# Kernel tuning notes

Hardware: AMD Instinct MI355X
Metric: run time of the kernel (lower is better)

The kernel has to match this reference:

```python
import jax, jax.numpy as jnp
import numpy as np

B, N, D_IN, D_OUT = 4, 4096, 512, 256
ALPHA = 0.2          # LeakyReLU negative slope
NEG_BIG = -9e15      # value used to mask non-edges before softmax


def setup_inputs() -> dict:
    key = jax.random.key(0)
    k_h, k_adj, k_w, k_a = jax.random.split(key, 4)
    h = jax.random.normal(k_h, (B, N, D_IN), dtype=jnp.float32)
    adj = jax.random.randint(k_adj, (N, N), 0, 2, dtype=jnp.int32)
    # xavier_uniform with gain 1.414
    lim_w = 1.414 * np.sqrt(6.0 / (D_IN + D_OUT))
    Ws = jax.random.uniform(k_w, (B, D_IN, D_OUT), jnp.float32, -lim_w, lim_w)
    lim_a = 1.414 * np.sqrt(6.0 / (2 * D_OUT + 1))
    a = jax.random.uniform(k_a, (B, 2 * D_OUT, 1), jnp.float32, -lim_a, lim_a)
    return {"h": h, "adj": adj, "Ws": Ws, "a": a}


def reference(h, adj, Ws, a):
    d_out = Ws.shape[-1]
    Wh = jnp.einsum('bni,bio->bno', h, Ws)                 # [B,N,D_OUT]
    a1 = a[:, :d_out, 0]                                    # [B,D_OUT]
    a2 = a[:, d_out:, 0]                                    # [B,D_OUT]
    e1 = jnp.einsum('bno,bo->bn', Wh, a1)                   # [B,N]
    e2 = jnp.einsum('bno,bo->bn', Wh, a2)                   # [B,N]
    e = e1[:, :, None] + e2[:, None, :]                     # [B,N,N]
    e = jnp.where(e > 0, e, ALPHA * e)                      # LeakyReLU
    scores = jnp.where(adj[None, :, :] > 0, e, NEG_BIG)     # mask non-edges
    att = jax.nn.softmax(scores, axis=-1)                   # over neighbors j
    # dropout omitted (eval mode / p irrelevant for correctness baseline)
    h_prime = jnp.einsum('bnm,bmo->bno', att, Wh)           # [B,N,D_OUT]
    return jax.nn.elu(h_prime)                              # concat=True -> elu
```

## Files before the change

### kernel.cpp

```cpp
#include <hip/hip_runtime.h>
#include <hip/hip_bf16.h>
#include <stdint.h>

#define B_    4
#define NN    4096
#define DIN   512
#define DOUT  256
#define ALPHA_ 0.2f

typedef __attribute__((ext_vector_type(8))) short short8;
typedef __attribute__((ext_vector_type(4))) float f32x4;
typedef __attribute__((ext_vector_type(2))) float f32x2;

typedef const __attribute__((address_space(1))) void gconst_void;
typedef __attribute__((address_space(3))) void lds_void;

__device__ __forceinline__ unsigned short f2bf(float x) {
    union { float f; uint32_t u; } v; v.f = x;
    uint32_t r = v.u + 0x7FFFu + ((v.u >> 16) & 1u);
    return (unsigned short)(r >> 16);
}

__global__ __launch_bounds__(256) void k_prep(const int* __restrict__ adj,
                                              const float4* __restrict__ h4,
                                              const float* __restrict__ Ws,
                                              uint32_t* __restrict__ bits,
                                              uint2* __restrict__ hb,
                                              unsigned short* __restrict__ wst) {
    const int gt = blockIdx.x * 256 + threadIdx.x;
    const int NT = 2048 * 256;
    for (int idx = gt; idx < NN * NN; idx += NT) {
        unsigned long long m = __ballot(adj[idx] > 0);
        if ((threadIdx.x & 63) == 0)
            *reinterpret_cast<unsigned long long*>(bits + ((idx >> 6) << 1)) = m;
    }
    for (int idx = gt; idx < B_ * NN * DIN / 4; idx += NT) {
        float4 v = h4[idx];
        uint2 o;
        o.x = (uint32_t)f2bf(v.x) | ((uint32_t)f2bf(v.y) << 16);
        o.y = (uint32_t)f2bf(v.z) | ((uint32_t)f2bf(v.w) << 16);
        hb[idx] = o;
    }
    for (int idx = gt; idx < B_ * DOUT * DIN; idx += NT) {
        int k = idx & (DIN - 1);
        int o = (idx >> 9) & (DOUT - 1);
        int b = idx >> 17;
        wst[idx] = f2bf(Ws[((size_t)b * DIN + k) * DOUT + o]);
    }
}

__global__ __launch_bounds__(256) void k_gemm1(const unsigned short* __restrict__ hb,
                                               const unsigned short* __restrict__ wst,
                                               const float* __restrict__ a,
                                               unsigned short* __restrict__ wht,
                                               float2* __restrict__ x1t,
                                               float* __restrict__ y1t,
                                               float* __restrict__ y2t) {
    __shared__ unsigned short Ah[64 * 64];
    __shared__ unsigned short Bw[256 * 64];
    __shared__ float e1s[64], e2s[64];
    const int tid = threadIdx.x;
    const int w = tid >> 6, lane = tid & 63;
    const int l15 = lane & 15, lhi = lane >> 4;
    const int b = blockIdx.y;
    const int n0 = blockIdx.x * 64;
    const unsigned short* hrow = hb + ((size_t)b * NN + n0) * DIN;
    const unsigned short* wrow = wst + (size_t)b * DOUT * DIN;

    if (tid < 64) { e1s[tid] = 0.f; e2s[tid] = 0.f; }

    f32x4 acc[4][4] = {};

    for (int kt = 0; kt < DIN / 64; ++kt) {
        const int k0 = kt * 64;
        #pragma unroll
        for (int it = 0; it < 2; ++it) {
            int q = it * 256 + tid;
            int row = q >> 3, c = q & 7;
            const unsigned short* src = hrow + (size_t)row * DIN + k0 + 8 * (c ^ (row & 7));
            char* dst = reinterpret_cast<char*>(Ah) + it * 4096 + w * 1024;
            __builtin_amdgcn_global_load_lds((gconst_void*)src, (lds_void*)dst, 16, 0, 0);
        }
        #pragma unroll
        for (int it = 0; it < 8; ++it) {
            int q = it * 256 + tid;
            int row = q >> 3, c = q & 7;
            const unsigned short* src = wrow + (size_t)row * DIN + k0 + 8 * (c ^ (row & 7));
            char* dst = reinterpret_cast<char*>(Bw) + it * 4096 + w * 1024;
            __builtin_amdgcn_global_load_lds((gconst_void*)src, (lds_void*)dst, 16, 0, 0);
        }
        __syncthreads();
        #pragma unroll
        for (int kk = 0; kk < 2; ++kk) {
            short8 af[4], bfr[4];
            #pragma unroll
            for (int rf = 0; rf < 4; ++rf) {
                int row = rf * 16 + l15;
                int off = row * 128 + ((kk * 64 + lhi * 16) ^ ((row & 7) << 4));
                af[rf] = *reinterpret_cast<const short8*>(reinterpret_cast<const char*>(Ah) + off);
            }
            #pragma unroll
            for (int cf = 0; cf < 4; ++cf) {
                int row = w * 64 + cf * 16 + l15;
                int off = row * 128 + ((kk * 64 + lhi * 16) ^ ((row & 7) << 4));
                bfr[cf] = *reinterpret_cast<const short8*>(reinterpret_cast<const char*>(Bw) + off);
            }
            #pragma unroll
            for (int rf = 0; rf < 4; ++rf)
                #pragma unroll
                for (int cf = 0; cf < 4; ++cf)
                    acc[rf][cf] = __builtin_amdgcn_mfma_f32_16x16x32_bf16(af[rf], bfr[cf], acc[rf][cf], 0, 0, 0);
        }
        __syncthreads();
    }
    unsigned short* wb = wht + (size_t)b * DOUT * NN;
    #pragma unroll
    for (int rf = 0; rf < 4; ++rf) {
        #pragma unroll
        for (int cf = 0; cf < 4; ++cf) {
            int d = w * 64 + cf * 16 + l15;
            int m = n0 + rf * 16 + lhi * 4;
            uint2 pk;
            pk.x = (uint32_t)f2bf(acc[rf][cf][0]) | ((uint32_t)f2bf(acc[rf][cf][1]) << 16);
            pk.y = (uint32_t)f2bf(acc[rf][cf][2]) | ((uint32_t)f2bf(acc[rf][cf][3]) << 16);
            *reinterpret_cast<uint2*>(wb + (size_t)d * NN + m) = pk;
        }
    }
    const float* ab = a + b * 2 * DOUT;
    float a1v[4], a2v[4];
    #pragma unroll
    for (int cf = 0; cf < 4; ++cf) {
        int d = w * 64 + cf * 16 + l15;
        a1v[cf] = ab[d];
        a2v[cf] = ab[DOUT + d];
    }
    #pragma unroll
    for (int rf = 0; rf < 4; ++rf) {
        #pragma unroll
        for (int j = 0; j < 4; ++j) {
            float p1 = 0.f, p2 = 0.f;
            #pragma unroll
            for (int cf = 0; cf < 4; ++cf) {
                p1 = fmaf(acc[rf][cf][j], a1v[cf], p1);
                p2 = fmaf(acc[rf][cf][j], a2v[cf], p2);
            }
            #pragma unroll
            for (int msk = 1; msk < 16; msk <<= 1) {
                p1 += __shfl_xor(p1, msk);
                p2 += __shfl_xor(p2, msk);
            }
            if (l15 == 0) {
                atomicAdd(&e1s[rf * 16 + lhi * 4 + j], p1);
                atomicAdd(&e2s[rf * 16 + lhi * 4 + j], p2);
            }
        }
    }
    __syncthreads();
    if (tid < 64) {
        float e1v = e1s[tid], e2v = e2s[tid];
        x1t[b * NN + n0 + tid] = float2{__expf(e1v), __expf(ALPHA_ * e1v)};
        y1t[b * NN + n0 + tid] = __expf(e2v);
        y2t[b * NN + n0 + tid] = __expf(ALPHA_ * e2v);
    }
}

__global__ __launch_bounds__(512, 4) void k_attn(const unsigned short* __restrict__ wht,
                                                 const uint32_t* __restrict__ bits,
                                                 const float2* __restrict__ x1t,
                                                 const float* __restrict__ y1t,
                                                 const float* __restrict__ y2t,
                                                 float* __restrict__ out,
                                                 float* __restrict__ part1,
                                                 float* __restrict__ sums0,
                                                 float* __restrict__ sums1) {
    __shared__ unsigned short Bw[2 * 256 * 64];
    __shared__ unsigned short Pt[2 * 64 * 64];

    const int tid = threadIdx.x;
    const int w = tid >> 6, lane = tid & 63;
    const int l15 = lane & 15, lh4 = lane >> 4;
    const int wn = w >> 2, wd = w & 3;

    const int bid = blockIdx.x;
    const int wg = ((bid & 7) << 6) | (bid >> 3);
    const int g  = wg >> 6;
    const int b  = g >> 1;
    const int n0 = ((g & 1) * 32 + (wg & 31)) << 6;
    const int T0 = ((wg >> 5) & 1) * 32;

    const int pr = tid >> 3, pc = tid & 7;
    const float2 xv = x1t[b * NN + n0 + pr];
    const float X1 = xv.x, X2 = xv.y;
    const unsigned short* wb = wht + (size_t)b * DOUT * NN;

    f32x4 acc[2][4] = {};
    f32x4 accs[2] = {};
    short8 ones;
    {
        union { short8 v; uint32_t u[4]; } ov;
        ov.u[0] = 0x3F803F80u; ov.u[1] = 0x3F803F80u;
        ov.u[2] = 0x3F803F80u; ov.u[3] = 0x3F803F80u;
        ones = ov.v;
    }

    const unsigned short* sp[4];
    #pragma unroll
    for (int it = 0; it < 4; ++it) {
        int q = it * 512 + tid;
        int row = q >> 3, c = q & 7;
        sp[it] = wb + (size_t)row * NN + T0 * 64 + 8 * (c ^ (row & 7));
    }
    const uint8_t* bp = reinterpret_cast<const uint8_t*>(bits) +
                        (size_t)(n0 + pr) * (NN / 8) + T0 * 8 + pc;
    const float4* y1p = reinterpret_cast<const float4*>(y1t + b * NN + T0 * 64 + pc * 8);
    const float4* y2p = reinterpret_cast<const float4*>(y2t + b * NN + T0 * 64 + pc * 8);

#define STAGE(BUF)                                                                     \
    {                                                                                  \
        _Pragma("unroll")                                                              \
        for (int it = 0; it < 4; ++it) {                                               \
            char* dst = reinterpret_cast<char*>(Bw) + (BUF) * 32768 + it * 8192 + w * 1024; \
            __builtin_amdgcn_global_load_lds((gconst_void*)sp[it], (lds_void*)dst, 16, 0, 0); \
            sp[it] += 64;                                                              \
        }                                                                              \
    }

#define P_MATH(BB, Y1A, Y1B, Y2A, Y2B, PKW)                                            \
    {                                                                                  \
        float v1[8] = {Y1A.x, Y1A.y, Y1A.z, Y1A.w, Y1B.x, Y1B.y, Y1B.z, Y1B.w};        \
        float v2[8] = {Y2A.x, Y2A.y, Y2A.z, Y2A.w, Y2B.x, Y2B.y, Y2B.z, Y2B.w};        \
        _Pragma("unroll")                                                              \
        for (int i = 0; i < 4; ++i) {                                                  \
            f32x2 pa = f32x2{v1[2 * i], v1[2 * i + 1]} * X1;                           \
            f32x2 pb = f32x2{v2[2 * i], v2[2 * i + 1]} * X2;                           \
            f32x2 pm = __builtin_elementwise_max(pa, pb);                              \
            union { __hip_bfloat162 h; uint32_t u; } cc;                               \
            cc.h = __float22bfloat162_rn(float2{pm.x, pm.y});                          \
            uint32_t b2 = ((BB) >> (2 * i)) & 3u;                                      \
            uint32_t mk = ((b2 & 1u) ? 0xFFFFu : 0u) | ((b2 & 2u) ? 0xFFFF0000u : 0u); \
            PKW[i] = cc.u & mk;                                                        \
        }                                                                              \
    }

#define PT_WRITE(PKW, BUF)                                                             \
    {                                                                                  \
        uint4 qv; qv.x = PKW[0]; qv.y = PKW[1]; qv.z = PKW[2]; qv.w = PKW[3];          \
        *reinterpret_cast<uint4*>(reinterpret_cast<char*>(Pt) + (BUF) * 8192 +         \
                                  pr * 128 + ((pc * 16) ^ ((pr & 7) << 4))) = qv;      \
    }

#define MM(CUR)                                                                        \
    {                                                                                  \
        const char* bwb = reinterpret_cast<const char*>(Bw) + (CUR) * 32768;           \
        const char* ptb = reinterpret_cast<const char*>(Pt) + (CUR) * 8192;            \
        __builtin_amdgcn_s_setprio(1);                                                 \
        _Pragma("unroll")                                                              \
        for (int kk = 0; kk < 2; ++kk) {                                               \
            short8 af[2], bf[4];                                                       \
            _Pragma("unroll")                                                          \
            for (int rf = 0; rf < 2; ++rf) {                                           \
                int row = wn * 32 + rf * 16 + l15;                                     \
                int off = row * 128 + ((kk * 64 + lh4 * 16) ^ ((row & 7) << 4));       \
                af[rf] = *reinterpret_cast<const short8*>(ptb + off);                  \
            }                                                                          \
            _Pragma("unroll")                                                          \
            for (int cf = 0; cf < 4; ++cf) {                                           \
                int row = wd * 64 + cf * 16 + l15;                                     \
                int off = row * 128 + ((kk * 64 + lh4 * 16) ^ ((row & 7) << 4));       \
                bf[cf] = *reinterpret_cast<const short8*>(bwb + off);                  \
            }                                                                          \
            _Pragma("unroll")                                                          \
            for (int rf = 0; rf < 2; ++rf) {                                           \
                _Pragma("unroll")                                                      \
                for (int cf = 0; cf < 4; ++cf)                                         \
                    acc[rf][cf] = __builtin_amdgcn_mfma_f32_16x16x32_bf16(             \
                        af[rf], bf[cf], acc[rf][cf], 0, 0, 0);                         \
                accs[rf] = __builtin_amdgcn_mfma_f32_16x16x32_bf16(                    \
                    af[rf], ones, accs[rf], 0, 0, 0);                                  \
            }                                                                          \
        }                                                                              \
        __builtin_amdgcn_s_setprio(0);                                                 \
    }

    STAGE(0)
    {
        uint32_t bb = *bp; bp += 8;
        float4 y1a = y1p[0], y1b = y1p[1]; y1p += 16;
        float4 y2a = y2p[0], y2b = y2p[1]; y2p += 16;
        uint32_t pkw[4];
        P_MATH(bb, y1a, y1b, y2a, y2b, pkw)
        PT_WRITE(pkw, 0)
    }
    __syncthreads();

    for (int t = 0; t < 32; ++t) {
        const int cur = t & 1;
        if (t < 31) {
            STAGE(cur ^ 1)
            uint32_t bb = *bp; bp += 8;
            float4 y1a = y1p[0], y1b = y1p[1]; y1p += 16;
            float4 y2a = y2p[0], y2b = y2p[1]; y2p += 16;
            uint32_t pkw[4];
            P_MATH(bb, y1a, y1b, y2a, y2b, pkw)
            PT_WRITE(pkw, cur ^ 1)
        }
        MM(cur)
        __syncthreads();
    }
#undef STAGE
#undef P_MATH
#undef PT_WRITE
#undef MM

    float* pdst = (T0 == 0) ? out : part1;
    #pragma unroll
    for (int rf = 0; rf < 2; ++rf) {
        #pragma unroll
        for (int cf = 0; cf < 4; ++cf) {
            int d = wd * 64 + cf * 16 + l15;
            #pragma unroll
            for (int j = 0; j < 4; ++j) {
                int nr = n0 + wn * 32 + rf * 16 + lh4 * 4 + j;
                pdst[((size_t)b * NN + nr) * DOUT + d] = acc[rf][cf][j];
            }
        }
    }
    if (wd == 0 && l15 == 0) {
        float* sdst = (T0 == 0) ? sums0 : sums1;
        #pragma unroll
        for (int rf = 0; rf < 2; ++rf)
            #pragma unroll
            for (int j = 0; j < 4; ++j) {
                int nr = n0 + wn * 32 + rf * 16 + lh4 * 4 + j;
                sdst[b * NN + nr] = accs[rf][j];
            }
    }
}

__global__ __launch_bounds__(256) void k_final(const float* __restrict__ part1,
                                               const float* __restrict__ sums0,
                                               const float* __restrict__ sums1,
                                               float* __restrict__ out) {
    int f4 = blockIdx.x * 256 + threadIdx.x;
    int row = f4 >> 6;
    float inv = 1.0f / (sums0[row] + sums1[row]);
    float4 v = reinterpret_cast<const float4*>(out)[f4];
    float4 p = reinterpret_cast<const float4*>(part1)[f4];
    v.x = (v.x + p.x) * inv;
    v.y = (v.y + p.y) * inv;
    v.z = (v.z + p.z) * inv;
    v.w = (v.w + p.w) * inv;
    v.x = v.x > 0.f ? v.x : (__expf(v.x) - 1.f);
    v.y = v.y > 0.f ? v.y : (__expf(v.y) - 1.f);
    v.z = v.z > 0.f ? v.z : (__expf(v.z) - 1.f);
    v.w = v.w > 0.f ? v.w : (__expf(v.w) - 1.f);
    reinterpret_cast<float4*>(out)[f4] = v;
}

extern "C" void kernel_launch(void* const* d_in, const int* in_sizes, int n_in,
                              void* d_out, int out_size, void* d_ws, size_t ws_size,
                              hipStream_t stream) {
    (void)in_sizes; (void)n_in; (void)out_size; (void)ws_size;
    const float* h   = (const float*)d_in[0];
    const int*   adj = (const int*)d_in[1];
    const float* Ws  = (const float*)d_in[2];
    const float* a   = (const float*)d_in[3];
    float* out = (float*)d_out;

    char* ws = (char*)d_ws;
    unsigned short* hb  = (unsigned short*)(ws);
    unsigned short* wst = (unsigned short*)(ws + 16777216);
    unsigned short* wht = (unsigned short*)(ws + 17825792);
    float2* x1t = (float2*)(ws + 26214400);
    float*  y1t = (float*)(ws + 26345472);
    float*  y2t = (float*)(ws + 26411008);
    uint32_t* bits = (uint32_t*)(ws + 26476544);
    float* sums0 = (float*)(ws + 28573696);
    float* sums1 = (float*)(ws + 28639232);
    float* part1 = (float*)hb;

    k_prep<<<dim3(2048), dim3(256), 0, stream>>>(adj, (const float4*)h, Ws,
                                                 bits, (uint2*)hb, wst);
    k_gemm1<<<dim3(NN / 64, B_), dim3(256), 0, stream>>>(hb, wst, a, wht, x1t, y1t, y2t);
    k_attn<<<dim3(512), dim3(512), 0, stream>>>(wht, bits, x1t, y1t, y2t,
                                                out, part1, sums0, sums1);
    k_final<<<dim3(B_ * NN * DOUT / 1024), dim3(256), 0, stream>>>(part1, sums0, sums1, out);
}
```

Before: 106.2 us.

## Fuse split-K reduction and ELU into attention kernel via last-arriver flag

Removes the separate finalize kernel: each pair of attention workgroups covering the same row tile writes its partial result and sums to scratch, then increments a per-pair atomic counter. The second workgroup to arrive reads the other's partial, normalizes, applies ELU and writes the output. This saves one launch and an extra read/write pass over the output. In exchange it adds a memset of the flags, threadfences, and a tail of extra work on half the workgroups, and both partials still go through global memory.

```diff
diff --git a/kernel.cpp b/kernel.cpp
--- a/kernel.cpp
+++ b/kernel.cpp
@@ -169,10 +169,12 @@
                                                  const float2* __restrict__ x1t,
                                                  const float* __restrict__ y1t,
                                                  const float* __restrict__ y2t,
-                                                 float* __restrict__ out,
+                                                 float* __restrict__ part0,
                                                  float* __restrict__ part1,
                                                  float* __restrict__ sums0,
-                                                 float* __restrict__ sums1) {
+                                                 float* __restrict__ sums1,
+                                                 int* __restrict__ flags,
+                                                 float* __restrict__ out) {
     __shared__ unsigned short Bw[2 * 256 * 64];
     __shared__ unsigned short Pt[2 * 64 * 64];
 
@@ -187,6 +189,7 @@
     const int b  = g >> 1;
     const int n0 = ((g & 1) * 32 + (wg & 31)) << 6;
     const int T0 = ((wg >> 5) & 1) * 32;
+    const int pairid = g * 32 + (wg & 31);
 
     const int pr = tid >> 3, pc = tid & 7;
     const float2 xv = x1t[b * NN + n0 + pr];
@@ -312,7 +315,7 @@
 #undef PT_WRITE
 #undef MM
 
-    float* pdst = (T0 == 0) ? out : part1;
+    float* pdst = (T0 == 0) ? part0 : part1;
     #pragma unroll
     for (int rf = 0; rf < 2; ++rf) {
         #pragma unroll
@@ -335,26 +338,37 @@
                 sdst[b * NN + nr] = accs[rf][j];
             }
     }
-}
-
-__global__ __launch_bounds__(256) void k_final(const float* __restrict__ part1,
-                                               const float* __restrict__ sums0,
-                                               const float* __restrict__ sums1,
-                                               float* __restrict__ out) {
-    int f4 = blockIdx.x * 256 + threadIdx.x;
-    int row = f4 >> 6;
-    float inv = 1.0f / (sums0[row] + sums1[row]);
-    float4 v = reinterpret_cast<const float4*>(out)[f4];
-    float4 p = reinterpret_cast<const float4*>(part1)[f4];
-    v.x = (v.x + p.x) * inv;
-    v.y = (v.y + p.y) * inv;
-    v.z = (v.z + p.z) * inv;
-    v.w = (v.w + p.w) * inv;
-    v.x = v.x > 0.f ? v.x : (__expf(v.x) - 1.f);
-    v.y = v.y > 0.f ? v.y : (__expf(v.y) - 1.f);
-    v.z = v.z > 0.f ? v.z : (__expf(v.z) - 1.f);
-    v.w = v.w > 0.f ? v.w : (__expf(v.w) - 1.f);
-    reinterpret_cast<float4*>(out)[f4] = v;
+
+    __threadfence();
+    int* lflag = reinterpret_cast<int*>(Pt);
+    if (tid == 0) *lflag = atomicAdd(&flags[pairid], 1);
+    __syncthreads();
+    if (*lflag == 1) {
+        __threadfence();
+        const float* ppart = (T0 == 0) ? part1 : part0;
+        const float* osums = (T0 == 0) ? sums1 : sums0;
+        #pragma unroll
+        for (int rf = 0; rf < 2; ++rf) {
+            float inv[4];
+            #pragma unroll
+            for (int j = 0; j < 4; ++j) {
+                int nr = n0 + wn * 32 + rf * 16 + lh4 * 4 + j;
+                inv[j] = 1.0f / (accs[rf][j] + osums[b * NN + nr]);
+            }
+            #pragma unroll
+            for (int cf = 0; cf < 4; ++cf) {
+                int d = wd * 64 + cf * 16 + l15;
+                #pragma unroll
+                for (int j = 0; j < 4; ++j) {
+                    int nr = n0 + wn * 32 + rf * 16 + lh4 * 4 + j;
+                    size_t idx = ((size_t)b * NN + nr) * DOUT + d;
+                    float x = (acc[rf][cf][j] + ppart[idx]) * inv[j];
+                    x = x > 0.f ? x : (__expf(x) - 1.f);
+                    out[idx] = x;
+                }
+            }
+        }
+    }
 }
 
 extern "C" void kernel_launch(void* const* d_in, const int* in_sizes, int n_in,
@@ -377,12 +391,14 @@
     uint32_t* bits = (uint32_t*)(ws + 26476544);
     float* sums0 = (float*)(ws + 28573696);
     float* sums1 = (float*)(ws + 28639232);
-    float* part1 = (float*)hb;
-
+    int*   flags = (int*)(ws + 28704768);
+    float* part0 = (float*)hb;
+    float* part1 = (float*)(ws + 28835840);
+
+    hipMemsetAsync(flags, 0, 1024, stream);
     k_prep<<<dim3(2048), dim3(256), 0, stream>>>(adj, (const float4*)h, Ws,
                                                  bits, (uint2*)hb, wst);
     k_gemm1<<<dim3(NN / 64, B_), dim3(256), 0, stream>>>(hb, wst, a, wht, x1t, y1t, y2t);
     k_attn<<<dim3(512), dim3(512), 0, stream>>>(wht, bits, x1t, y1t, y2t,
-                                                out, part1, sums0, sums1);
-    k_final<<<dim3(B_ * NN * DOUT / 1024), dim3(256), 0, stream>>>(part1, sums0, sums1, out);
+                                                part0, part1, sums0, sums1, flags, out);
 }
```

After: 285.0 us. +168.4%, slower.
